# Optimization experiments

Hardware: AMD Instinct MI355X
Metric: run time of the kernel (lower is better)

The kernel has to match this reference:

```python
import jax, jax.numpy as jnp
import numpy as np

# ---- geometry / physics constants (from init_kwargs) ----
nx, NX = 96, 192
dx, nt, dt = 1.0, 200, 0.3
nm, sr, sR = 32, 4, 70
fc, sgma, t0, bg = 0.5, 1.0, 3.0, 1.5
abc_pd = NX // 2 - sR - 1          # 25
pd = (NX - nx) // 2 - abc_pd       # 23
TOT = pd + abc_pd                  # total pad on each side

_thetas = 2 * np.pi * np.arange(nm) / nm
_mx = (NX / 2 + sR * np.cos(_thetas)).astype(int)
_my = (NX / 2 + sR * np.sin(_thetas)).astype(int)
MEAS = jnp.asarray(NX * _mx + _my)            # (nm,) flat receiver indices
TRANS = jnp.asarray((NX * _mx + _my)[::sr])   # (nr,) flat source indices
NR = int(TRANS.shape[0])                      # 8 source channels

_times = np.arange(nt) * dt
SRC = jnp.asarray(np.sin(2 * np.pi * fc * _times) * np.exp(-(_times - t0) ** 2 / (2 * sgma ** 2)), dtype=jnp.float32)

# background field: bg everywhere except outer abc ring of width abc_pd = 1e-6
_bgf = np.full((NX, NX), 1e-6, dtype=np.float32)
_bgf[abc_pd:-abc_pd, abc_pd:-abc_pd] = bg
BGF = jnp.asarray(_bgf)[None, None]           # (1,1,NX,NX)


def lap4(p):
    """4th-order 5-point stencil Laplacian with periodic (roll) wrap, matching torch.roll."""
    r = lambda s, a: jnp.roll(p, s, axis=a)
    lx = (-r(2, -2) + 16 * r(1, -2) - 30 * p + 16 * r(-1, -2) - r(-2, -2)) / 12
    ly = (-r(2, -1) + 16 * r(1, -1) - 30 * p + 16 * r(-1, -1) - r(-2, -1)) / 12
    return lx + ly


def compute_P0():
    """HelperFoward on the homogeneous bg medium: background wavefield (1,NR,nt,NX,NX)."""
    coef = (dt * BGF / dx) ** 2
    amp = (bg * dt / dx) ** 2
    ch = jnp.arange(NR)

    def step(carry, s):
        p0, p1 = carry
        p = 2 * p1 - p0 + coef * lap4(p1)
        pf = p.reshape(1, NR, NX * NX)
        pf = pf.at[:, ch, TRANS].add(amp * s)   # one source pixel per channel (eye)
        p = pf.reshape(1, NR, NX, NX)
        return (p1, p), p

    z = jnp.zeros((1, NR, NX, NX), jnp.float32)
    _, ps = jax.lax.scan(step, (z, z), SRC)      # (nt,1,NR,NX,NX)
    return jnp.transpose(ps, (1, 2, 0, 3, 4))    # (1,NR,nt,NX,NX)


def setup_inputs() -> dict:
    key = jax.random.key(0)
    # sound-speed map around bg=1.5 (must be positive; module computes bg/x)
    x = bg + 0.1 * (jax.random.uniform(key, (2, 1, nx, nx), jnp.float32) - 0.5)
    P0 = compute_P0()
    return {"x": x, "P0": P0}


def reference(x, P0):
    B = x.shape[0]
    xx = bg / x
    # both pads use value 1 -> single constant pad of width TOT
    X = jnp.pad(xx, ((0, 0), (0, 0), (TOT, TOT), (TOT, TOT)), constant_values=1.0)
    coef = (dt * BGF / dx) ** 2                          # (1,1,NX,NX)
    rf = (BGF / bg) ** 2 * (1.0 - X ** 2)                # (B,1,NX,NX)
    # second time-difference of the background field; zero for j<2
    P0t = jnp.transpose(P0, (2, 0, 1, 3, 4))             # (nt,1,NR,NX,NX)
    d2 = jnp.zeros_like(P0t).at[2:].set(P0t[2:] - 2 * P0t[1:-1] + P0t[:-2])

    def step(carry, d2j):
        p0, p1 = carry
        p = 2 * p1 - p0 + coef * lap4(p1) + rf * d2j     # (B,NR,NX,NX)
        meas = p.reshape(B, NR, NX * NX)[:, :, MEAS]     # (B,NR,nm)
        return (p1, p), meas

    z = jnp.zeros((B, NR, NX, NX), x.dtype)
    _, outs = jax.lax.scan(step, (z, z), d2)             # (nt,B,NR,nm)
    return jnp.transpose(outs, (1, 2, 3, 0))             # (B,NR,nm,nt)
```

## Files before the change

### kernel.cpp

```cpp
#include <hip/hip_runtime.h>
#include <math.h>

#define NXg      192
#define PLANE_SZ (NXg*NXg)
#define PLANES   16
#define TOTAL    (PLANES*PLANE_SZ)
#define NT       200
#define NM       32
#define CW       96
#define C0       48
#define W96SQ    (CW*CW)
#define A0       24
#define TILE     36
#define HALO     20
#define EXPW     76
#define LSTR     84
#define KSTEP    10
#define NLAUNCH  20
#define NSB      (38*19)
#define BLK      768

struct MeasIdx { int v[NM]; };
typedef float4 f4;
typedef float2 f2;

__global__ void rf_kernel(const float* __restrict__ x, float* __restrict__ rf){
    int i = blockIdx.x*blockDim.x + threadIdx.x;
    if (i < 2*W96SQ){ float t = 1.5f/x[i]; rf[i] = 1.0f - t*t; }
}

__device__ __forceinline__ f4 frow(f2 L, f4 C, f2 Q,
                                   f4 m2, f4 m1, f4 p1, f4 p2,
                                   f4 O, f4 CF, f4 RF, f4 D2)
{
    const float s = 1.0f/12.0f;
    float v0=L.x, v1=L.y, v2=C.x, v3=C.y, v4=C.z, v5=C.w, v6=Q.x, v7=Q.y;
    float lxA = (-v0 + 16.f*v1 - 30.f*v2 + 16.f*v3 - v4)*s;
    float lxB = (-v1 + 16.f*v2 - 30.f*v3 + 16.f*v4 - v5)*s;
    float lxC = (-v2 + 16.f*v3 - 30.f*v4 + 16.f*v5 - v6)*s;
    float lxD = (-v3 + 16.f*v4 - 30.f*v5 + 16.f*v6 - v7)*s;
    float lyA = (-m2.x + 16.f*m1.x - 30.f*v2 + 16.f*p1.x - p2.x)*s;
    float lyB = (-m2.y + 16.f*m1.y - 30.f*v3 + 16.f*p1.y - p2.y)*s;
    float lyC = (-m2.z + 16.f*m1.z - 30.f*v4 + 16.f*p1.z - p2.z)*s;
    float lyD = (-m2.w + 16.f*m1.w - 30.f*v5 + 16.f*p1.w - p2.w)*s;
    f4 r;
    r.x = 2.f*v2 - O.x + CF.x*(lxA+lyA) + RF.x*D2.x;
    r.y = 2.f*v3 - O.y + CF.y*(lxB+lyB) + RF.y*D2.y;
    r.z = 2.f*v4 - O.z + CF.z*(lxC+lyC) + RF.z*D2.z;
    r.w = 2.f*v5 - O.w + CF.w*(lxD+lyD) + RF.w*D2.w;
    return r;
}

__device__ __forceinline__ f4 d2c(f4 c, f4 b, f4 a){
    f4 r;
    r.x = c.x - 2.f*b.x + a.x;
    r.y = c.y - 2.f*b.y + a.y;
    r.z = c.z - 2.f*b.z + a.z;
    r.w = c.w - 2.f*b.w + a.w;
    return r;
}

__global__ __launch_bounds__(BLK, 3)
void step_fused(const float* __restrict__ RA, const float* __restrict__ RB,
                float* __restrict__ WA, float* __restrict__ WB,
                const float* __restrict__ P0, const float* __restrict__ rf,
                float* __restrict__ out, int J, MeasIdx meas)
{
    __shared__ float lds0[EXPW*LSTR];
    __shared__ float lds1[EXPW*LSTR];
    const int tid = threadIdx.x;
    const int sw  = ((blockIdx.x & 7) << 5) | (blockIdx.x >> 3);
    const int pl  = sw >> 4;
    const int t   = sw & 15;
    const int ty  = t >> 2, tx = t & 3;
    const int gy0 = A0 + ty*TILE - HALO;
    const int gx0 = A0 + tx*TILE - HALO;
    const int b   = pl >> 3, rch = pl & 7;
    const size_t pbase = (size_t)pl * PLANE_SZ;

    for (int i = tid; i < EXPW*19; i += BLK){
        int ly = i/19, lx4 = (i%19)*4;
        size_t go = pbase + (size_t)(gy0+ly)*NXg + (gx0+lx4);
        *(f4*)&lds0[ly*LSTR + lx4] = *(const f4*)&RA[go];
        *(f4*)&lds1[ly*LSTR + lx4] = *(const f4*)&RB[go];
    }

    const bool val = (tid < NSB);
    const int gg  = val ? tid : 0;
    const int sby = gg/19, sbx = gg%19;
    const int ly0 = 2*sby, lx0 = 4*sbx;
    const int oC  = ly0*LSTR + lx0;
    int s1 = (ly0-1) >> 1;
    int s2 = (73-ly0) >> 1;
    int s3 = (lx0+1) >> 1;
    int s4 = (73-lx0) >> 1;
    const int sMax = val ? min(min(s1,s2), min(s3,s4)) : -1;
    const int gy = gy0 + ly0, gx = gx0 + lx0;
    const bool win = (gy>=C0 && gy<C0+CW && gx>=C0 && gx<C0+CW);
    const int pofs = win ? (gy*NXg + gx) : 0;

    f4 rfa, rfb2;
    if (win){
        const float* rp = rf + ((size_t)b*CW + (gy-C0))*CW + (gx-C0);
        rfa  = *(const f4*)rp;
        rfb2 = *(const f4*)(rp + CW);
    } else {
        rfa = make_float4(0.f,0.f,0.f,0.f);
        rfb2 = rfa;
    }
    f4 cfa, cfb;
    {
        float c0v[4], c1v[4];
#pragma unroll
        for (int ii=0; ii<4; ++ii){
            int gxr = gx + ii;
            bool ix = (gxr>=25 && gxr<167);
            float g0 = 0.3f * ((ix && gy  >=25 && gy  <167) ? 1.5f : 1e-6f);
            float g1 = 0.3f * ((ix && gy+1>=25 && gy+1<167) ? 1.5f : 1e-6f);
            c0v[ii] = g0*g0;
            c1v[ii] = g1*g1;
        }
        cfa = make_float4(c0v[0],c0v[1],c0v[2],c0v[3]);
        cfb = make_float4(c1v[0],c1v[1],c1v[2],c1v[3]);
    }

    bool own = false; int loff = 0; size_t obase = 0;
    if (tid < NM){
        int rv = meas.v[tid];
        int ry = rv / NXg, rx = rv % NXg;
        int dy = ry - (A0 + ty*TILE), dx = rx - (A0 + tx*TILE);
        own = ((unsigned)dy < TILE) && ((unsigned)dx < TILE);
        loff = (dy+HALO)*LSTR + (dx+HALO);
        obase = ((size_t)pl*NM + tid)*NT;
    }

    const float* P0r = P0 + (size_t)rch*NT*PLANE_SZ;
    f4 z4 = make_float4(0.f,0.f,0.f,0.f);
    f4 Pa0=z4, Pa1=z4, Pb0=z4, Pb1=z4, D0=z4, D1=z4;
    if (win){
        const float* p = P0r + (size_t)J*PLANE_SZ + pofs;
        Pa0 = *(const f4*)p;
        Pa1 = *(const f4*)(p + NXg);
        if (J >= 1){
            Pb0 = *(const f4*)(p - PLANE_SZ);
            Pb1 = *(const f4*)(p - PLANE_SZ + NXg);
        }
        if (J >= 2){
            f4 Pc0 = *(const f4*)(p - 2*PLANE_SZ);
            f4 Pc1 = *(const f4*)(p - 2*PLANE_SZ + NXg);
            D0 = d2c(Pa0, Pb0, Pc0);
            D1 = d2c(Pa1, Pb1, Pc1);
        }
    }

    __syncthreads();

    f4 OA0 = *(const f4*)&lds0[oC];
    f4 OA1 = *(const f4*)&lds0[oC+LSTR];
    f4 OB0 = *(const f4*)&lds1[oC];
    f4 OB1 = *(const f4*)&lds1[oC+LSTR];

#pragma unroll
    for (int s=0; s<KSTEP; ++s){
        float* pa = (s&1) ? lds1 : lds0;
        float* pb = (s&1) ? lds0 : lds1;

        const bool pre = (s+1 < KSTEP) && win && ((s+1) <= sMax);
        f4 Pn0 = z4, Pn1 = z4;
        if (pre){
            const float* p = P0r + (size_t)(J+s+1)*PLANE_SZ + pofs;
            Pn0 = *(const f4*)p;
            Pn1 = *(const f4*)(p + NXg);
        }

        if (s <= sMax){
            f4 C0r = (s&1) ? OA0 : OB0;
            f4 C1r = (s&1) ? OA1 : OB1;
            f4 O0  = (s&1) ? OB0 : OA0;
            f4 O1  = (s&1) ? OB1 : OA1;
            f4 Rm2 = *(const f4*)&pb[oC - 2*LSTR];
            f4 Rm1 = *(const f4*)&pb[oC -   LSTR];
            f4 Rp2 = *(const f4*)&pb[oC + 2*LSTR];
            f4 Rp3 = *(const f4*)&pb[oC + 3*LSTR];
            f2 L0  = *(const f2*)&pb[oC - 2];
            f2 L1  = *(const f2*)&pb[oC + LSTR - 2];
            f2 Q0  = *(const f2*)&pb[oC + 4];
            f2 Q1  = *(const f2*)&pb[oC + LSTR + 4];
            f4 N0 = frow(L0, C0r, Q0, Rm2, Rm1, C1r, Rp2, O0, cfa, rfa,  D0);
            f4 N1 = frow(L1, C1r, Q1, Rm1, C0r, Rp2, Rp3, O1, cfb, rfb2, D1);
            *(f4*)&pa[oC]        = N0;
            *(f4*)&pa[oC + LSTR] = N1;
            if (s&1){ OB0=N0; OB1=N1; } else { OA0=N0; OA1=N1; }
        }

        if (pre){
            if (J+s+1 >= 2){
                D0 = d2c(Pn0, Pa0, Pb0);
                D1 = d2c(Pn1, Pa1, Pb1);
            } else {
                D0 = z4; D1 = z4;
            }
            Pb0 = Pa0; Pb1 = Pa1;
            Pa0 = Pn0; Pa1 = Pn1;
        }

        __syncthreads();
        if (own) out[obase + (J+s)] = pa[loff];
    }

    for (int i = tid; i < TILE*(TILE/4); i += BLK){
        int r = i/9, c4 = (i%9)*4;
        size_t go = pbase + (size_t)(A0 + ty*TILE + r)*NXg + (A0 + tx*TILE + c4);
        int lo = (r+HALO)*LSTR + (c4+HALO);
        *(f4*)&WB[go] = *(const f4*)&lds1[lo];
        *(f4*)&WA[go] = *(const f4*)&lds0[lo];
    }
}

extern "C" void kernel_launch(void* const* d_in, const int* in_sizes, int n_in,
                              void* d_out, int out_size, void* d_ws, size_t ws_size,
                              hipStream_t stream)
{
    const float* x  = (const float*)d_in[0];
    const float* P0 = (const float*)d_in[1];
    float* out = (float*)d_out;

    float* F   = (float*)d_ws;
    float* f0  = F;
    float* f1  = F + (size_t)TOTAL;
    float* f2p = F + 2*(size_t)TOTAL;
    float* f3p = F + 3*(size_t)TOTAL;
    float* rfb = F + 4*(size_t)TOTAL;

    hipMemsetAsync(F, 0, (size_t)4*TOTAL*sizeof(float), stream);

    rf_kernel<<<(2*W96SQ+255)/256, 256, 0, stream>>>(x, rfb);

    MeasIdx meas;
    for (int k=0;k<NM;++k){
        double th = 2.0*M_PI*(double)k/(double)NM;
        int mx = (int)(96.0 + 70.0*cos(th));
        int my = (int)(96.0 + 70.0*sin(th));
        meas.v[k] = mx*NXg + my;
    }

    float *RA=f0, *RB=f1, *WA=f2p, *WB=f3p;
    for (int L=0; L<NLAUNCH; ++L){
        step_fused<<<256, BLK, 0, stream>>>(RA,RB,WA,WB,P0,rfb,out,L*KSTEP,meas);
        float* tsw;
        tsw=RA; RA=WA; WA=tsw;
        tsw=RB; RB=WB; WB=tsw;
    }
}
```

Before: 237.2 us.

## Fuse chunk launches into one persistent kernel with neighbor-tile flag sync

Replaces the 20 sequential kernel launches with a single persistent kernel that loops over the time chunks. Between chunks, each block waits on per-tile acquire/release flags set by its up to 8 neighbouring tiles, instead of relying on a full kernel boundary. Because a tile's own 36x36 interior stays in LDS, each chunk reloads only the halo ring from global memory. Oversized dynamic LDS forces one block per CU, and correctness depends on all 256 blocks being resident at once, otherwise the spin-waits deadlock.

```diff
diff --git a/kernel.cpp b/kernel.cpp
--- a/kernel.cpp
+++ b/kernel.cpp
@@ -16,9 +16,12 @@
 #define EXPW     76
 #define LSTR     84
 #define KSTEP    10
-#define NLAUNCH  20
+#define NCH      20
 #define NSB      (38*19)
 #define BLK      768
+#define LDS_FLOATS (EXPW*LSTR)
+#define LDS_FORCE  86016
+#define NRING    1120
 
 struct MeasIdx { int v[NM]; };
 typedef float4 f4;
@@ -61,13 +64,15 @@
 }
 
 __global__ __launch_bounds__(BLK, 3)
-void step_fused(const float* __restrict__ RA, const float* __restrict__ RB,
-                float* __restrict__ WA, float* __restrict__ WB,
-                const float* __restrict__ P0, const float* __restrict__ rf,
-                float* __restrict__ out, int J, MeasIdx meas)
+void born_persist(const float* __restrict__ P0, const float* __restrict__ rf,
+                  float* __restrict__ out,
+                  float* __restrict__ f0, float* __restrict__ f1,
+                  float* __restrict__ f2p, float* __restrict__ f3p,
+                  int* flags, MeasIdx meas)
 {
-    __shared__ float lds0[EXPW*LSTR];
-    __shared__ float lds1[EXPW*LSTR];
+    extern __shared__ float ldsraw[];
+    float* lds0 = ldsraw;
+    float* lds1 = ldsraw + LDS_FLOATS;
     const int tid = threadIdx.x;
     const int sw  = ((blockIdx.x & 7) << 5) | (blockIdx.x >> 3);
     const int pl  = sw >> 4;
@@ -78,11 +83,18 @@
     const int b   = pl >> 3, rch = pl & 7;
     const size_t pbase = (size_t)pl * PLANE_SZ;
 
-    for (int i = tid; i < EXPW*19; i += BLK){
-        int ly = i/19, lx4 = (i%19)*4;
-        size_t go = pbase + (size_t)(gy0+ly)*NXg + (gx0+lx4);
-        *(f4*)&lds0[ly*LSTR + lx4] = *(const f4*)&RA[go];
-        *(f4*)&lds1[ly*LSTR + lx4] = *(const f4*)&RB[go];
+    int myNb = -1;
+    if (tid < 8){
+        int cnt = 0;
+        for (int dy=-1; dy<=1; ++dy)
+        for (int dx=-1; dx<=1; ++dx){
+            if (!dy && !dx) continue;
+            int ny = ty+dy, nx = tx+dx;
+            if ((unsigned)ny < 4u && (unsigned)nx < 4u){
+                if (cnt == tid) myNb = (pl<<4) + (ny<<2) + nx;
+                cnt++;
+            }
+        }
     }
 
     const bool val = (tid < NSB);
@@ -135,85 +147,120 @@
     }
 
     const float* P0r = P0 + (size_t)rch*NT*PLANE_SZ;
-    f4 z4 = make_float4(0.f,0.f,0.f,0.f);
-    f4 Pa0=z4, Pa1=z4, Pb0=z4, Pb1=z4, D0=z4, D1=z4;
-    if (win){
-        const float* p = P0r + (size_t)J*PLANE_SZ + pofs;
-        Pa0 = *(const f4*)p;
-        Pa1 = *(const f4*)(p + NXg);
-        if (J >= 1){
-            Pb0 = *(const f4*)(p - PLANE_SZ);
-            Pb1 = *(const f4*)(p - PLANE_SZ + NXg);
-        }
-        if (J >= 2){
-            f4 Pc0 = *(const f4*)(p - 2*PLANE_SZ);
-            f4 Pc1 = *(const f4*)(p - 2*PLANE_SZ + NXg);
-            D0 = d2c(Pa0, Pb0, Pc0);
-            D1 = d2c(Pa1, Pb1, Pc1);
-        }
-    }
-
-    __syncthreads();
-
-    f4 OA0 = *(const f4*)&lds0[oC];
-    f4 OA1 = *(const f4*)&lds0[oC+LSTR];
-    f4 OB0 = *(const f4*)&lds1[oC];
-    f4 OB1 = *(const f4*)&lds1[oC+LSTR];
+    const f4 z4 = make_float4(0.f,0.f,0.f,0.f);
+
+#pragma unroll 1
+    for (int ch=0; ch<NCH; ++ch){
+        const int J = ch*KSTEP;
+        const float* RA = (ch&1) ? f2p : f0;
+        const float* RB = (ch&1) ? f3p : f1;
+        float*       WA = (ch&1) ? f0  : f2p;
+        float*       WB = (ch&1) ? f1  : f3p;
+
+        if (ch > 0 && myNb >= 0){
+            while (__hip_atomic_load(&flags[myNb], __ATOMIC_ACQUIRE,
+                                     __HIP_MEMORY_SCOPE_AGENT) < ch)
+                __builtin_amdgcn_s_sleep(4);
+        }
+        __syncthreads();
+
+        if (ch == 0){
+            for (int i = tid; i < 2*LDS_FLOATS; i += BLK) ldsraw[i] = 0.f;
+        } else {
+            for (int i = tid; i < NRING; i += BLK){
+                int ly, lx4;
+                if (i < 380){ ly = i/19;            lx4 = (i%19)*4; }
+                else if (i < 760){ int k=i-380; ly = 56 + k/19; lx4 = (k%19)*4; }
+                else { int k=i-760; ly = 20 + k/10; int m=k%10; lx4 = (m<5)? m*4 : 36+m*4; }
+                size_t go = pbase + (size_t)(gy0+ly)*NXg + (gx0+lx4);
+                *(f4*)&lds0[ly*LSTR + lx4] = *(const f4*)&RA[go];
+                *(f4*)&lds1[ly*LSTR + lx4] = *(const f4*)&RB[go];
+            }
+        }
+
+        f4 Pa0=z4, Pa1=z4, Pb0=z4, Pb1=z4, D0=z4, D1=z4;
+        if (win){
+            const float* p = P0r + (size_t)J*PLANE_SZ + pofs;
+            Pa0 = *(const f4*)p;
+            Pa1 = *(const f4*)(p + NXg);
+            if (J >= 1){
+                Pb0 = *(const f4*)(p - PLANE_SZ);
+                Pb1 = *(const f4*)(p - PLANE_SZ + NXg);
+            }
+            if (J >= 2){
+                f4 Pc0 = *(const f4*)(p - 2*PLANE_SZ);
+                f4 Pc1 = *(const f4*)(p - 2*PLANE_SZ + NXg);
+                D0 = d2c(Pa0, Pb0, Pc0);
+                D1 = d2c(Pa1, Pb1, Pc1);
+            }
+        }
+
+        __syncthreads();
+
+        f4 OA0 = *(const f4*)&lds0[oC];
+        f4 OA1 = *(const f4*)&lds0[oC+LSTR];
+        f4 OB0 = *(const f4*)&lds1[oC];
+        f4 OB1 = *(const f4*)&lds1[oC+LSTR];
 
 #pragma unroll
-    for (int s=0; s<KSTEP; ++s){
-        float* pa = (s&1) ? lds1 : lds0;
-        float* pb = (s&1) ? lds0 : lds1;
-
-        const bool pre = (s+1 < KSTEP) && win && ((s+1) <= sMax);
-        f4 Pn0 = z4, Pn1 = z4;
-        if (pre){
-            const float* p = P0r + (size_t)(J+s+1)*PLANE_SZ + pofs;
-            Pn0 = *(const f4*)p;
-            Pn1 = *(const f4*)(p + NXg);
-        }
-
-        if (s <= sMax){
-            f4 C0r = (s&1) ? OA0 : OB0;
-            f4 C1r = (s&1) ? OA1 : OB1;
-            f4 O0  = (s&1) ? OB0 : OA0;
-            f4 O1  = (s&1) ? OB1 : OA1;
-            f4 Rm2 = *(const f4*)&pb[oC - 2*LSTR];
-            f4 Rm1 = *(const f4*)&pb[oC -   LSTR];
-            f4 Rp2 = *(const f4*)&pb[oC + 2*LSTR];
-            f4 Rp3 = *(const f4*)&pb[oC + 3*LSTR];
-            f2 L0  = *(const f2*)&pb[oC - 2];
-            f2 L1  = *(const f2*)&pb[oC + LSTR - 2];
-            f2 Q0  = *(const f2*)&pb[oC + 4];
-            f2 Q1  = *(const f2*)&pb[oC + LSTR + 4];
-            f4 N0 = frow(L0, C0r, Q0, Rm2, Rm1, C1r, Rp2, O0, cfa, rfa,  D0);
-            f4 N1 = frow(L1, C1r, Q1, Rm1, C0r, Rp2, Rp3, O1, cfb, rfb2, D1);
-            *(f4*)&pa[oC]        = N0;
-            *(f4*)&pa[oC + LSTR] = N1;
-            if (s&1){ OB0=N0; OB1=N1; } else { OA0=N0; OA1=N1; }
-        }
-
-        if (pre){
-            if (J+s+1 >= 2){
-                D0 = d2c(Pn0, Pa0, Pb0);
-                D1 = d2c(Pn1, Pa1, Pb1);
-            } else {
-                D0 = z4; D1 = z4;
-            }
-            Pb0 = Pa0; Pb1 = Pa1;
-            Pa0 = Pn0; Pa1 = Pn1;
-        }
-
-        __syncthreads();
-        if (own) out[obase + (J+s)] = pa[loff];
-    }
-
-    for (int i = tid; i < TILE*(TILE/4); i += BLK){
-        int r = i/9, c4 = (i%9)*4;
-        size_t go = pbase + (size_t)(A0 + ty*TILE + r)*NXg + (A0 + tx*TILE + c4);
-        int lo = (r+HALO)*LSTR + (c4+HALO);
-        *(f4*)&WB[go] = *(const f4*)&lds1[lo];
-        *(f4*)&WA[go] = *(const f4*)&lds0[lo];
+        for (int s=0; s<KSTEP; ++s){
+            float* pa = (s&1) ? lds1 : lds0;
+            float* pb = (s&1) ? lds0 : lds1;
+
+            const bool pre = (s+1 < KSTEP) && win && ((s+1) <= sMax);
+            f4 Pn0 = z4, Pn1 = z4;
+            if (pre){
+                const float* p = P0r + (size_t)(J+s+1)*PLANE_SZ + pofs;
+                Pn0 = *(const f4*)p;
+                Pn1 = *(const f4*)(p + NXg);
+            }
+
+            if (s <= sMax){
+                f4 C0r = (s&1) ? OA0 : OB0;
+                f4 C1r = (s&1) ? OA1 : OB1;
+                f4 O0  = (s&1) ? OB0 : OA0;
+                f4 O1  = (s&1) ? OB1 : OA1;
+                f4 Rm2 = *(const f4*)&pb[oC - 2*LSTR];
+                f4 Rm1 = *(const f4*)&pb[oC -   LSTR];
+                f4 Rp2 = *(const f4*)&pb[oC + 2*LSTR];
+                f4 Rp3 = *(const f4*)&pb[oC + 3*LSTR];
+                f2 L0  = *(const f2*)&pb[oC - 2];
+                f2 L1  = *(const f2*)&pb[oC + LSTR - 2];
+                f2 Q0  = *(const f2*)&pb[oC + 4];
+                f2 Q1  = *(const f2*)&pb[oC + LSTR + 4];
+                f4 N0 = frow(L0, C0r, Q0, Rm2, Rm1, C1r, Rp2, O0, cfa, rfa,  D0);
+                f4 N1 = frow(L1, C1r, Q1, Rm1, C0r, Rp2, Rp3, O1, cfb, rfb2, D1);
+                *(f4*)&pa[oC]        = N0;
+                *(f4*)&pa[oC + LSTR] = N1;
+                if (s&1){ OB0=N0; OB1=N1; } else { OA0=N0; OA1=N1; }
+            }
+
+            if (pre){
+                if (J+s+1 >= 2){
+                    D0 = d2c(Pn0, Pa0, Pb0);
+                    D1 = d2c(Pn1, Pa1, Pb1);
+                } else { D0 = z4; D1 = z4; }
+                Pb0 = Pa0; Pb1 = Pa1;
+                Pa0 = Pn0; Pa1 = Pn1;
+            }
+
+            __syncthreads();
+            if (own) out[obase + (J+s)] = pa[loff];
+        }
+
+        if (ch < NCH-1){
+            for (int i = tid; i < TILE*(TILE/4); i += BLK){
+                int r = i/9, c4 = (i%9)*4;
+                size_t go = pbase + (size_t)(A0 + ty*TILE + r)*NXg + (A0 + tx*TILE + c4);
+                int lo = (r+HALO)*LSTR + (c4+HALO);
+                *(f4*)&WB[go] = *(const f4*)&lds1[lo];
+                *(f4*)&WA[go] = *(const f4*)&lds0[lo];
+            }
+            __syncthreads();
+            if (tid == 0)
+                __hip_atomic_store(&flags[sw], ch+1, __ATOMIC_RELEASE,
+                                   __HIP_MEMORY_SCOPE_AGENT);
+        }
     }
 }
 
@@ -231,8 +278,10 @@
     float* f2p = F + 2*(size_t)TOTAL;
     float* f3p = F + 3*(size_t)TOTAL;
     float* rfb = F + 4*(size_t)TOTAL;
-
-    hipMemsetAsync(F, 0, (size_t)4*TOTAL*sizeof(float), stream);
+    int*  flags = (int*)(rfb + 2*W96SQ);
+
+    size_t zbytes = ((size_t)4*TOTAL + 2*W96SQ)*sizeof(float) + 256*sizeof(int);
+    hipMemsetAsync(d_ws, 0, zbytes, stream);
 
     rf_kernel<<<(2*W96SQ+255)/256, 256, 0, stream>>>(x, rfb);
 
@@ -244,11 +293,6 @@
         meas.v[k] = mx*NXg + my;
     }
 
-    float *RA=f0, *RB=f1, *WA=f2p, *WB=f3p;
-    for (int L=0; L<NLAUNCH; ++L){
-        step_fused<<<256, BLK, 0, stream>>>(RA,RB,WA,WB,P0,rfb,out,L*KSTEP,meas);
-        float* tsw;
-        tsw=RA; RA=WA; WA=tsw;
-        tsw=RB; RB=WB; WB=tsw;
-    }
-}
+    born_persist<<<256, BLK, LDS_FORCE, stream>>>(P0, rfb, out,
+                                                  f0, f1, f2p, f3p, flags, meas);
+}
```

New measurement: 431.0 us. 81.7% more time.

## Drop memset and rf kernel, zero-fill halo in-kernel, fold stencil scale into coef

Applied to the files above, without the earlier changes.

Removes the workspace memset and separate rf kernel by computing rf from x inside the step kernel and zero-filling the LDS tile on the first launch and outside the written region. The stencil is rewritten with FMAs and the 1/12 factor folded into the coefficient, cutting ALU work per point. Saves two launches and memset traffic, at the cost of extra divisions per thread per launch and reliance on never-written workspace regions being masked out.

```diff
diff --git a/kernel.cpp b/kernel.cpp
--- a/kernel.cpp
+++ b/kernel.cpp
@@ -24,30 +24,47 @@
 typedef float4 f4;
 typedef float2 f2;
 
-__global__ void rf_kernel(const float* __restrict__ x, float* __restrict__ rf){
-    int i = blockIdx.x*blockDim.x + threadIdx.x;
-    if (i < 2*W96SQ){ float t = 1.5f/x[i]; rf[i] = 1.0f - t*t; }
-}
-
-__device__ __forceinline__ f4 frow(f2 L, f4 C, f2 Q,
-                                   f4 m2, f4 m1, f4 p1, f4 p2,
-                                   f4 O, f4 CF, f4 RF, f4 D2)
+__device__ __forceinline__ f4 frow2(f2 L, f4 C, f2 Q,
+                                    f4 m2, f4 m1, f4 p1, f4 p2,
+                                    f4 O, f4 CFs, f4 RF, f4 D2)
 {
-    const float s = 1.0f/12.0f;
-    float v0=L.x, v1=L.y, v2=C.x, v3=C.y, v4=C.z, v5=C.w, v6=Q.x, v7=Q.y;
-    float lxA = (-v0 + 16.f*v1 - 30.f*v2 + 16.f*v3 - v4)*s;
-    float lxB = (-v1 + 16.f*v2 - 30.f*v3 + 16.f*v4 - v5)*s;
-    float lxC = (-v2 + 16.f*v3 - 30.f*v4 + 16.f*v5 - v6)*s;
-    float lxD = (-v3 + 16.f*v4 - 30.f*v5 + 16.f*v6 - v7)*s;
-    float lyA = (-m2.x + 16.f*m1.x - 30.f*v2 + 16.f*p1.x - p2.x)*s;
-    float lyB = (-m2.y + 16.f*m1.y - 30.f*v3 + 16.f*p1.y - p2.y)*s;
-    float lyC = (-m2.z + 16.f*m1.z - 30.f*v4 + 16.f*p1.z - p2.z)*s;
-    float lyD = (-m2.w + 16.f*m1.w - 30.f*v5 + 16.f*p1.w - p2.w)*s;
     f4 r;
-    r.x = 2.f*v2 - O.x + CF.x*(lxA+lyA) + RF.x*D2.x;
-    r.y = 2.f*v3 - O.y + CF.y*(lxB+lyB) + RF.y*D2.y;
-    r.z = 2.f*v4 - O.z + CF.z*(lxC+lyC) + RF.z*D2.z;
-    r.w = 2.f*v5 - O.w + CF.w*(lxD+lyD) + RF.w*D2.w;
+    {
+        float s16 = (L.y + C.y) + (m1.x + p1.x);
+        float s1  = (L.x + C.z) + (m2.x + p2.x);
+        float st  = fmaf(16.f, s16, -s1);
+        st = fmaf(-60.f, C.x, st);
+        float p = fmaf(2.f, C.x, -O.x);
+        p = fmaf(CFs.x, st, p);
+        r.x = fmaf(RF.x, D2.x, p);
+    }
+    {
+        float s16 = (C.x + C.z) + (m1.y + p1.y);
+        float s1  = (L.y + C.w) + (m2.y + p2.y);
+        float st  = fmaf(16.f, s16, -s1);
+        st = fmaf(-60.f, C.y, st);
+        float p = fmaf(2.f, C.y, -O.y);
+        p = fmaf(CFs.y, st, p);
+        r.y = fmaf(RF.y, D2.y, p);
+    }
+    {
+        float s16 = (C.y + C.w) + (m1.z + p1.z);
+        float s1  = (C.x + Q.x) + (m2.z + p2.z);
+        float st  = fmaf(16.f, s16, -s1);
+        st = fmaf(-60.f, C.z, st);
+        float p = fmaf(2.f, C.z, -O.z);
+        p = fmaf(CFs.z, st, p);
+        r.z = fmaf(RF.z, D2.z, p);
+    }
+    {
+        float s16 = (C.z + Q.x) + (m1.w + p1.w);
+        float s1  = (C.y + Q.y) + (m2.w + p2.w);
+        float st  = fmaf(16.f, s16, -s1);
+        st = fmaf(-60.f, C.w, st);
+        float p = fmaf(2.f, C.w, -O.w);
+        p = fmaf(CFs.w, st, p);
+        r.w = fmaf(RF.w, D2.w, p);
+    }
     return r;
 }
 
@@ -63,7 +80,7 @@
 __global__ __launch_bounds__(BLK, 3)
 void step_fused(const float* __restrict__ RA, const float* __restrict__ RB,
                 float* __restrict__ WA, float* __restrict__ WB,
-                const float* __restrict__ P0, const float* __restrict__ rf,
+                const float* __restrict__ P0, const float* __restrict__ x,
                 float* __restrict__ out, int J, MeasIdx meas)
 {
     __shared__ float lds0[EXPW*LSTR];
@@ -77,12 +94,25 @@
     const int gx0 = A0 + tx*TILE - HALO;
     const int b   = pl >> 3, rch = pl & 7;
     const size_t pbase = (size_t)pl * PLANE_SZ;
-
-    for (int i = tid; i < EXPW*19; i += BLK){
-        int ly = i/19, lx4 = (i%19)*4;
-        size_t go = pbase + (size_t)(gy0+ly)*NXg + (gx0+lx4);
-        *(f4*)&lds0[ly*LSTR + lx4] = *(const f4*)&RA[go];
-        *(f4*)&lds1[ly*LSTR + lx4] = *(const f4*)&RB[go];
+    const f4 z4 = make_float4(0.f,0.f,0.f,0.f);
+
+    {
+        const bool zf = (J == 0);
+        for (int i = tid; i < EXPW*19; i += BLK){
+            int ly = i/19, lx4 = (i%19)*4;
+            int gyr = gy0 + ly, gxg = gx0 + lx4;
+            bool ok = !zf && ((unsigned)(gyr - A0) < 144u)
+                          && ((unsigned)(gxg - A0) < 144u);
+            f4 va = z4, vb = z4;
+            if (ok){
+                size_t go = pbase + (size_t)gyr*NXg + gxg;
+                va = *(const f4*)&RA[go];
+                vb = *(const f4*)&RB[go];
+            }
+            int lo = ly*LSTR + lx4;
+            *(f4*)&lds0[lo] = va;
+            *(f4*)&lds1[lo] = vb;
+        }
     }
 
     const bool val = (tid < NSB);
@@ -101,12 +131,20 @@
 
     f4 rfa, rfb2;
     if (win){
-        const float* rp = rf + ((size_t)b*CW + (gy-C0))*CW + (gx-C0);
-        rfa  = *(const f4*)rp;
-        rfb2 = *(const f4*)(rp + CW);
+        const float* xp = x + (size_t)b*W96SQ + (size_t)(gy-C0)*CW + (gx-C0);
+        f4 x0 = *(const f4*)xp;
+        f4 x1 = *(const f4*)(xp + CW);
+        float tq;
+        tq = 1.5f/x0.x; rfa.x  = 1.0f - tq*tq;
+        tq = 1.5f/x0.y; rfa.y  = 1.0f - tq*tq;
+        tq = 1.5f/x0.z; rfa.z  = 1.0f - tq*tq;
+        tq = 1.5f/x0.w; rfa.w  = 1.0f - tq*tq;
+        tq = 1.5f/x1.x; rfb2.x = 1.0f - tq*tq;
+        tq = 1.5f/x1.y; rfb2.y = 1.0f - tq*tq;
+        tq = 1.5f/x1.z; rfb2.z = 1.0f - tq*tq;
+        tq = 1.5f/x1.w; rfb2.w = 1.0f - tq*tq;
     } else {
-        rfa = make_float4(0.f,0.f,0.f,0.f);
-        rfb2 = rfa;
+        rfa = z4; rfb2 = z4;
     }
     f4 cfa, cfb;
     {
@@ -117,8 +155,8 @@
             bool ix = (gxr>=25 && gxr<167);
             float g0 = 0.3f * ((ix && gy  >=25 && gy  <167) ? 1.5f : 1e-6f);
             float g1 = 0.3f * ((ix && gy+1>=25 && gy+1<167) ? 1.5f : 1e-6f);
-            c0v[ii] = g0*g0;
-            c1v[ii] = g1*g1;
+            c0v[ii] = (g0*g0)*(1.0f/12.0f);
+            c1v[ii] = (g1*g1)*(1.0f/12.0f);
         }
         cfa = make_float4(c0v[0],c0v[1],c0v[2],c0v[3]);
         cfb = make_float4(c1v[0],c1v[1],c1v[2],c1v[3]);
@@ -135,7 +173,6 @@
     }
 
     const float* P0r = P0 + (size_t)rch*NT*PLANE_SZ;
-    f4 z4 = make_float4(0.f,0.f,0.f,0.f);
     f4 Pa0=z4, Pa1=z4, Pb0=z4, Pb1=z4, D0=z4, D1=z4;
     if (win){
         const float* p = P0r + (size_t)J*PLANE_SZ + pofs;
@@ -186,8 +223,8 @@
             f2 L1  = *(const f2*)&pb[oC + LSTR - 2];
             f2 Q0  = *(const f2*)&pb[oC + 4];
             f2 Q1  = *(const f2*)&pb[oC + LSTR + 4];
-            f4 N0 = frow(L0, C0r, Q0, Rm2, Rm1, C1r, Rp2, O0, cfa, rfa,  D0);
-            f4 N1 = frow(L1, C1r, Q1, Rm1, C0r, Rp2, Rp3, O1, cfb, rfb2, D1);
+            f4 N0 = frow2(L0, C0r, Q0, Rm2, Rm1, C1r, Rp2, O0, cfa, rfa,  D0);
+            f4 N1 = frow2(L1, C1r, Q1, Rm1, C0r, Rp2, Rp3, O1, cfb, rfb2, D1);
             *(f4*)&pa[oC]        = N0;
             *(f4*)&pa[oC + LSTR] = N1;
             if (s&1){ OB0=N0; OB1=N1; } else { OA0=N0; OA1=N1; }
@@ -197,9 +234,7 @@
             if (J+s+1 >= 2){
                 D0 = d2c(Pn0, Pa0, Pb0);
                 D1 = d2c(Pn1, Pa1, Pb1);
-            } else {
-                D0 = z4; D1 = z4;
-            }
+            } else { D0 = z4; D1 = z4; }
             Pb0 = Pa0; Pb1 = Pa1;
             Pa0 = Pn0; Pa1 = Pn1;
         }
@@ -230,11 +265,7 @@
     float* f1  = F + (size_t)TOTAL;
     float* f2p = F + 2*(size_t)TOTAL;
     float* f3p = F + 3*(size_t)TOTAL;
-    float* rfb = F + 4*(size_t)TOTAL;
-
-    hipMemsetAsync(F, 0, (size_t)4*TOTAL*sizeof(float), stream);
-
-    rf_kernel<<<(2*W96SQ+255)/256, 256, 0, stream>>>(x, rfb);
+
 
     MeasIdx meas;
     for (int k=0;k<NM;++k){
@@ -246,7 +277,7 @@
 
     float *RA=f0, *RB=f1, *WA=f2p, *WB=f3p;
     for (int L=0; L<NLAUNCH; ++L){
-        step_fused<<<256, BLK, 0, stream>>>(RA,RB,WA,WB,P0,rfb,out,L*KSTEP,meas);
+        step_fused<<<256, BLK, 0, stream>>>(RA,RB,WA,WB,P0,x,out,L*KSTEP,meas);
         float* tsw;
         tsw=RA; RA=WA; WA=tsw;
         tsw=RB; RB=WB; WB=tsw;
```

Result: no change. 232.9 us (-1.8%).
